# Optimization experiments

Measured on AMD Instinct MI355X. Metric: run time of the kernel, lower is better.

The kernel has to match this reference:

```python
import jax, jax.numpy as jnp
import numpy as np

SCALE = 0.125  # quantization scale applied inline in the custom matmul
PAD = 4
STRIDE = 1


def setup_inputs() -> dict:
    key = jax.random.key(0)
    k1, k2, k3 = jax.random.split(key, 3)
    x = jax.random.normal(k1, (8, 64, 16384), dtype=jnp.float32)        # (N, C, L)
    weight = jax.random.normal(k2, (64, 64, 9), dtype=jnp.float32) * 0.05  # (O, I, K)
    bias = jax.random.normal(k3, (64,), dtype=jnp.float32)               # (O,)
    return {"x": x, "weight": weight, "bias": bias}


def reference(x, weight, bias):
    # Mathematically identical to: im2col unfold -> (N, out_l, C*K) @ (C*K, O),
    # then out * scale + bias. Expressed as a fused conv to avoid the huge
    # intermediate while computing the same result.
    out = jax.lax.conv_general_dilated(
        x, weight,
        window_strides=(STRIDE,),
        padding=[(PAD, PAD)],
        dimension_numbers=("NCH", "OIH", "NCH"),
    )  # (N, O, out_l)
    return out * SCALE + bias[None, :, None]
```

## Files before the change

kernel.cpp:

```cpp
#include <hip/hip_runtime.h>
#include <hip/hip_bf16.h>

#define C_IN    64
#define L_IN    16384
#define O_OUT   64
#define KTAP    9
#define LTILE   256
#define ROWS    272
#define RSTRIDE 72

typedef short          bf16x8 __attribute__((ext_vector_type(8)));
typedef unsigned int   u32x4  __attribute__((ext_vector_type(4)));
typedef float          f32x4  __attribute__((ext_vector_type(4)));

static __device__ __forceinline__ unsigned short f2bf(float f) {
  __hip_bfloat16 h = __float2bfloat16(f);
  return __builtin_bit_cast(unsigned short, h);
}

static __device__ __forceinline__ unsigned int pk2(float lo, float hi) {
  return (unsigned int)f2bf(lo) | ((unsigned int)f2bf(hi) << 16);
}

__global__ void w_rearrange(const float* __restrict__ w,
                            unsigned short* __restrict__ w2) {
    int i = blockIdx.x * 256 + threadIdx.x;
    if (i >= KTAP * O_OUT * C_IN) return;
    int t  = i >> 12;
    int oc = i & 4095;
    w2[i] = f2bf(w[oc * KTAP + t] * 0.125f);
}

__global__ __launch_bounds__(256) void qconv_kernel(
    const float* __restrict__ x,
    const unsigned short* __restrict__ w2,
    const float* __restrict__ bias,
    float* __restrict__ out) {

  __shared__ __align__(16) unsigned short xs[ROWS][RSTRIDE];

  const int tid = threadIdx.x;
  const int n   = blockIdx.x >> 6;
  const int l0  = (blockIdx.x & 63) << 8;
  const float* xn = x + (size_t)n * C_IN * L_IN;

  const int ucb = tid & 7;
  const int ulb = tid >> 3;
  const int uc0 = ucb << 3;

  const int a0_gl0 = l0 - 8 + (ulb << 2);
  const bool a0_ok = (a0_gl0 >= 0) && (a0_gl0 + 4 <= L_IN);
  f32x4 va0[8];
  if (a0_ok) {
#pragma unroll
    for (int i = 0; i < 8; ++i)
      va0[i] = *reinterpret_cast<const f32x4*>(xn + (size_t)(uc0 + i) * L_IN + a0_gl0);
  }
  const bool have1 = (tid < 32);
  const int a1_gl0 = l0 - 8 + ((32 + ulb) << 2);
  f32x4 va1[8];
  if (have1) {
#pragma unroll
    for (int i = 0; i < 8; ++i)
      va1[i] = *reinterpret_cast<const f32x4*>(xn + (size_t)(uc0 + i) * L_IN + a1_gl0);
  }
  const int b_gl0 = l0 + 136 + (ulb << 2);
  const bool b_ok = (b_gl0 + 4 <= L_IN);
  f32x4 vb[8];
  if (b_ok) {
#pragma unroll
    for (int i = 0; i < 8; ++i)
      vb[i] = *reinterpret_cast<const f32x4*>(xn + (size_t)(uc0 + i) * L_IN + b_gl0);
  }

  if (a0_ok) {
#pragma unroll
    for (int j = 0; j < 4; ++j) {
      u32x4 wv;
#pragma unroll
      for (int p = 0; p < 4; ++p)
        wv[p] = pk2(va0[2 * p][j], va0[2 * p + 1][j]);
      *reinterpret_cast<u32x4*>(&xs[(ulb << 2) + j][uc0]) = wv;
    }
  } else {
#pragma unroll
    for (int j = 0; j < 4; ++j) {
      const int gl = a0_gl0 + j;
      u32x4 wv;
#pragma unroll
      for (int p = 0; p < 4; ++p) {
        float lo = 0.f, hi = 0.f;
        if (gl >= 0 && gl < L_IN) {
          lo = xn[(size_t)(uc0 + 2 * p)     * L_IN + gl];
          hi = xn[(size_t)(uc0 + 2 * p + 1) * L_IN + gl];
        }
        wv[p] = pk2(lo, hi);
      }
      *reinterpret_cast<u32x4*>(&xs[(ulb << 2) + j][uc0]) = wv;
    }
  }
  if (have1) {
#pragma unroll
    for (int j = 0; j < 4; ++j) {
      u32x4 wv;
#pragma unroll
      for (int p = 0; p < 4; ++p)
        wv[p] = pk2(va1[2 * p][j], va1[2 * p + 1][j]);
      *reinterpret_cast<u32x4*>(&xs[128 + (ulb << 2) + j][uc0]) = wv;
    }
  }
  __syncthreads();

  const int wave = tid >> 6;
  const int lane = tid & 63;
  const int col  = lane & 15;
  const int quad = lane >> 4;

  const unsigned short* wbase = w2 + (((wave << 4) + col) << 6) + (quad << 3);
  const int obase = (wave << 4) + (quad << 2);
  float bv[4];
#pragma unroll
  for (int reg = 0; reg < 4; ++reg) bv[reg] = bias[obase + reg];

  f32x4 acc[8];
#pragma unroll
  for (int lt = 0; lt < 8; ++lt) acc[lt] = (f32x4){0.f, 0.f, 0.f, 0.f};

  for (int t = 0; t < KTAP; ++t) {
    bf16x8 a[2];
#pragma unroll
    for (int k = 0; k < 2; ++k)
      a[k] = *reinterpret_cast<const bf16x8*>(wbase + (t << 12) + (k << 5));
#pragma unroll
    for (int k = 0; k < 2; ++k) {
#pragma unroll
      for (int lt = 0; lt < 8; ++lt) {
        const int r = col + t + 4 + (lt << 4);
        const bf16x8 b = *reinterpret_cast<const bf16x8*>(&xs[r][(k << 5) + (quad << 3)]);
        acc[lt] = __builtin_amdgcn_mfma_f32_16x16x32_bf16(a[k], b, acc[lt], 0, 0, 0);
      }
    }
  }

  if (b_ok) {
#pragma unroll
    for (int j = 0; j < 4; ++j) {
      u32x4 wv;
#pragma unroll
      for (int p = 0; p < 4; ++p)
        wv[p] = pk2(vb[2 * p][j], vb[2 * p + 1][j]);
      *reinterpret_cast<u32x4*>(&xs[144 + (ulb << 2) + j][uc0]) = wv;
    }
  } else {
#pragma unroll
    for (int j = 0; j < 4; ++j) {
      const int gl = b_gl0 + j;
      u32x4 wv;
#pragma unroll
      for (int p = 0; p < 4; ++p) {
        float lo = 0.f, hi = 0.f;
        if (gl < L_IN) {
          lo = xn[(size_t)(uc0 + 2 * p)     * L_IN + gl];
          hi = xn[(size_t)(uc0 + 2 * p + 1) * L_IN + gl];
        }
        wv[p] = pk2(lo, hi);
      }
      *reinterpret_cast<u32x4*>(&xs[144 + (ulb << 2) + j][uc0]) = wv;
    }
  }
  __syncthreads();

#pragma unroll
  for (int lt = 0; lt < 8; ++lt) {
    const int l = l0 + (lt << 4) + col;
#pragma unroll
    for (int reg = 0; reg < 4; ++reg)
      out[((size_t)(n * O_OUT + obase + reg) << 14) + l] = acc[lt][reg] + bv[reg];
  }

#pragma unroll
  for (int lt = 0; lt < 8; ++lt) acc[lt] = (f32x4){0.f, 0.f, 0.f, 0.f};

  for (int t = 0; t < KTAP; ++t) {
    bf16x8 a[2];
#pragma unroll
    for (int k = 0; k < 2; ++k)
      a[k] = *reinterpret_cast<const bf16x8*>(wbase + (t << 12) + (k << 5));
#pragma unroll
    for (int k = 0; k < 2; ++k) {
#pragma unroll
      for (int lt = 0; lt < 8; ++lt) {
        const int r = 128 + col + t + 4 + (lt << 4);
        const bf16x8 b = *reinterpret_cast<const bf16x8*>(&xs[r][(k << 5) + (quad << 3)]);
        acc[lt] = __builtin_amdgcn_mfma_f32_16x16x32_bf16(a[k], b, acc[lt], 0, 0, 0);
      }
    }
  }

#pragma unroll
  for (int lt = 0; lt < 8; ++lt) {
    const int l = l0 + 128 + (lt << 4) + col;
#pragma unroll
    for (int reg = 0; reg < 4; ++reg)
      out[((size_t)(n * O_OUT + obase + reg) << 14) + l] = acc[lt][reg] + bv[reg];
  }
}

extern "C" void kernel_launch(void* const* d_in, const int* in_sizes, int n_in,
                              void* d_out, int out_size, void* d_ws, size_t ws_size,
                              hipStream_t stream) {
  const float*    x    = (const float*)d_in[0];
  const float*    w    = (const float*)d_in[1];
  const float*    bias = (const float*)d_in[2];
  float*          out  = (float*)d_out;
  unsigned short* w2   = (unsigned short*)d_ws;

  w_rearrange<<<(KTAP * O_OUT * C_IN + 255) / 256, 256, 0, stream>>>(w, w2);

  qconv_kernel<<<8 * (L_IN / LTILE), 256, 0, stream>>>(x, w2, bias, out);

  qconv_kernel<<<8 * (L_IN / LTILE), 256, 0, stream>>>(x, w2, bias, out);
}
```

Baseline: 118.4 us.

## Retile waves to 32x64 output blocks and drop the duplicate conv launch

Each wave's output tile changes from 16 channels by 128 positions to 32 channels by 64 positions, so every LDS-loaded input fragment now feeds two MFMAs. This halves shared-memory reads per MFMA. The weight fragments loaded per tap double, and accumulator register use stays about the same. The second, identical launch of the conv kernel, which only recomputed the same output, is also removed.

```diff
diff --git a/kernel.cpp b/kernel.cpp
--- a/kernel.cpp
+++ b/kernel.cpp
@@ -113,31 +113,41 @@
 
   const int wave = tid >> 6;
   const int lane = tid & 63;
+  const int wr   = wave >> 1;
+  const int wq   = wave & 1;
   const int col  = lane & 15;
   const int quad = lane >> 4;
 
-  const unsigned short* wbase = w2 + (((wave << 4) + col) << 6) + (quad << 3);
-  const int obase = (wave << 4) + (quad << 2);
-  float bv[4];
-#pragma unroll
-  for (int reg = 0; reg < 4; ++reg) bv[reg] = bias[obase + reg];
-
-  f32x4 acc[8];
-#pragma unroll
-  for (int lt = 0; lt < 8; ++lt) acc[lt] = (f32x4){0.f, 0.f, 0.f, 0.f};
-
+  const int obase = (wr << 5) + (quad << 2);
+  float bv[2][4];
+#pragma unroll
+  for (int m = 0; m < 2; ++m)
+#pragma unroll
+    for (int reg = 0; reg < 4; ++reg) bv[m][reg] = bias[obase + (m << 4) + reg];
+
+  f32x4 acc[2][4];
+#pragma unroll
+  for (int m = 0; m < 2; ++m)
+#pragma unroll
+    for (int lt = 0; lt < 4; ++lt) acc[m][lt] = (f32x4){0.f, 0.f, 0.f, 0.f};
+
+  const int rbaseA = (wq << 6) + col + 4;
   for (int t = 0; t < KTAP; ++t) {
-    bf16x8 a[2];
-#pragma unroll
-    for (int k = 0; k < 2; ++k)
-      a[k] = *reinterpret_cast<const bf16x8*>(wbase + (t << 12) + (k << 5));
+    bf16x8 a[2][2];
+#pragma unroll
+    for (int m = 0; m < 2; ++m)
+#pragma unroll
+      for (int k = 0; k < 2; ++k)
+        a[m][k] = *reinterpret_cast<const bf16x8*>(
+            w2 + (t << 12) + (((wr << 5) + (m << 4) + col) << 6) + (k << 5) + (quad << 3));
 #pragma unroll
     for (int k = 0; k < 2; ++k) {
 #pragma unroll
-      for (int lt = 0; lt < 8; ++lt) {
-        const int r = col + t + 4 + (lt << 4);
+      for (int lt = 0; lt < 4; ++lt) {
+        const int r = rbaseA + t + (lt << 4);
         const bf16x8 b = *reinterpret_cast<const bf16x8*>(&xs[r][(k << 5) + (quad << 3)]);
-        acc[lt] = __builtin_amdgcn_mfma_f32_16x16x32_bf16(a[k], b, acc[lt], 0, 0, 0);
+        acc[0][lt] = __builtin_amdgcn_mfma_f32_16x16x32_bf16(a[0][k], b, acc[0][lt], 0, 0, 0);
+        acc[1][lt] = __builtin_amdgcn_mfma_f32_16x16x32_bf16(a[1][k], b, acc[1][lt], 0, 0, 0);
       }
     }
   }
@@ -171,38 +181,52 @@
   __syncthreads();
 
 #pragma unroll
-  for (int lt = 0; lt < 8; ++lt) {
-    const int l = l0 + (lt << 4) + col;
-#pragma unroll
-    for (int reg = 0; reg < 4; ++reg)
-      out[((size_t)(n * O_OUT + obase + reg) << 14) + l] = acc[lt][reg] + bv[reg];
-  }
-
-#pragma unroll
-  for (int lt = 0; lt < 8; ++lt) acc[lt] = (f32x4){0.f, 0.f, 0.f, 0.f};
+  for (int m = 0; m < 2; ++m) {
+#pragma unroll
+    for (int lt = 0; lt < 4; ++lt) {
+      const int l = l0 + (wq << 6) + (lt << 4) + col;
+#pragma unroll
+      for (int reg = 0; reg < 4; ++reg)
+        out[((size_t)(n * O_OUT + obase + (m << 4) + reg) << 14) + l] =
+            acc[m][lt][reg] + bv[m][reg];
+    }
+  }
+
+#pragma unroll
+  for (int m = 0; m < 2; ++m)
+#pragma unroll
+    for (int lt = 0; lt < 4; ++lt) acc[m][lt] = (f32x4){0.f, 0.f, 0.f, 0.f};
 
   for (int t = 0; t < KTAP; ++t) {
-    bf16x8 a[2];
-#pragma unroll
-    for (int k = 0; k < 2; ++k)
-      a[k] = *reinterpret_cast<const bf16x8*>(wbase + (t << 12) + (k << 5));
+    bf16x8 a[2][2];
+#pragma unroll
+    for (int m = 0; m < 2; ++m)
+#pragma unroll
+      for (int k = 0; k < 2; ++k)
+        a[m][k] = *reinterpret_cast<const bf16x8*>(
+            w2 + (t << 12) + (((wr << 5) + (m << 4) + col) << 6) + (k << 5) + (quad << 3));
 #pragma unroll
     for (int k = 0; k < 2; ++k) {
 #pragma unroll
-      for (int lt = 0; lt < 8; ++lt) {
-        const int r = 128 + col + t + 4 + (lt << 4);
+      for (int lt = 0; lt < 4; ++lt) {
+        const int r = 128 + rbaseA + t + (lt << 4);
         const bf16x8 b = *reinterpret_cast<const bf16x8*>(&xs[r][(k << 5) + (quad << 3)]);
-        acc[lt] = __builtin_amdgcn_mfma_f32_16x16x32_bf16(a[k], b, acc[lt], 0, 0, 0);
-      }
-    }
-  }
-
-#pragma unroll
-  for (int lt = 0; lt < 8; ++lt) {
-    const int l = l0 + 128 + (lt << 4) + col;
-#pragma unroll
-    for (int reg = 0; reg < 4; ++reg)
-      out[((size_t)(n * O_OUT + obase + reg) << 14) + l] = acc[lt][reg] + bv[reg];
+        acc[0][lt] = __builtin_amdgcn_mfma_f32_16x16x32_bf16(a[0][k], b, acc[0][lt], 0, 0, 0);
+        acc[1][lt] = __builtin_amdgcn_mfma_f32_16x16x32_bf16(a[1][k], b, acc[1][lt], 0, 0, 0);
+      }
+    }
+  }
+
+#pragma unroll
+  for (int m = 0; m < 2; ++m) {
+#pragma unroll
+    for (int lt = 0; lt < 4; ++lt) {
+      const int l = l0 + 128 + (wq << 6) + (lt << 4) + col;
+#pragma unroll
+      for (int reg = 0; reg < 4; ++reg)
+        out[((size_t)(n * O_OUT + obase + (m << 4) + reg) << 14) + l] =
+            acc[m][lt][reg] + bv[m][reg];
+    }
   }
 }
 
@@ -218,6 +242,4 @@
   w_rearrange<<<(KTAP * O_OUT * C_IN + 255) / 256, 256, 0, stream>>>(w, w2);
 
   qconv_kernel<<<8 * (L_IN / LTILE), 256, 0, stream>>>(x, w2, bias, out);
-
-  qconv_kernel<<<8 * (L_IN / LTILE), 256, 0, stream>>>(x, w2, bias, out);
-}
+}
```

Measured after the change: 104.3 us. -11.9%, faster.
